# Kernel tuning notes

Hardware: AMD Instinct MI355X
Metric: run time of the kernel (lower is better)

Reference implementation:

```python
import jax, jax.numpy as jnp
import numpy as np

KS = 7          # kernel_size
DIL = 1         # dilation
NUM_ITER = 10   # num_iterations
K2 = KS * KS
CENTER = K2 // 2  # self position removed from window


def _sliding_window(x):
    # x: [B, C, H, W] -> [B, C, K2-1, H, W], replicate-padded local windows
    pad = (KS - 1) * DIL // 2
    B, C, H, W = x.shape
    xp = jnp.pad(x, ((0, 0), (0, 0), (pad, pad), (pad, pad)), mode='edge')
    wins = [xp[:, :, i * DIL:i * DIL + H, j * DIL:j * DIL + W]
            for i in range(KS) for j in range(KS)]
    wins = wins[:CENTER] + wins[CENTER + 1:]  # remove_self=True
    return jnp.stack(wins, axis=2)


def _local_affinity(x):
    # x: [B, C, H, W] -> softmax-normalized affinity [B, 1, K2-1, H, W]
    q = x[:, :, None]                 # [B, C, 1, H, W]
    k = _sliding_window(x)            # [B, C, K2-1, H, W]
    std = jnp.std(k, axis=2, keepdims=True, ddof=1)  # torch .std is unbiased
    aff = -jnp.abs(k - q) / (1e-8 + 0.1 * std)
    aff = jnp.mean(aff, axis=1, keepdims=True)       # [B, 1, K2-1, H, W]
    return jax.nn.softmax(aff, axis=2)


def setup_inputs() -> dict:
    key = jax.random.key(0)
    k1, k2 = jax.random.split(key)
    feats = jax.random.normal(k1, (4, 3, 128, 128), dtype=jnp.float32)
    mask = jax.random.uniform(k2, (4, 21, 128, 128), dtype=jnp.float32)
    return {"feats": feats, "mask": mask}


def reference(feats, mask):
    aff = _local_affinity(feats)  # [B, 1, K2-1, H, W]

    def body(m, _):
        v = _sliding_window(m)            # [B, Cm, K2-1, H, W]
        return (v * aff).sum(axis=2), None

    mask, _ = jax.lax.scan(body, mask, None, length=NUM_ITER)
    return mask
```

## Files before the change

### kernel.cpp

```cpp
#include <hip/hip_runtime.h>

constexpr int B   = 4;
constexpr int CF  = 3;
constexpr int CM  = 21;
constexpr int H   = 128;
constexpr int W   = 128;
constexpr int KS  = 7;
constexpr int PAD = 3;
constexpr int CENTER = (KS * KS) / 2;
constexpr int NNB = KS * KS - 1;
constexpr int NUM_ITER = 10;

constexpr int TILE = 16;
constexpr int TH   = TILE + 2 * PAD;
constexpr int TS   = 24;
constexpr int HW   = H * W;

constexpr int IN   = TILE + 4 * PAD;
constexpr int IND  = 15;
constexpr int MD   = 22;
constexpr int MDD  = 12;
constexpr int CPB  = 7;
constexpr int INP  = CPB * IN * IND;
constexpr int MDP  = CPB * MD * MDD;

__device__ __forceinline__ unsigned short f2b(float v) {
    unsigned int x = __float_as_uint(v);
    x += 0x7fffu + ((x >> 16) & 1u);
    return (unsigned short)(x >> 16);
}
__device__ __forceinline__ float blo(unsigned int d) { return __uint_as_float(d << 16); }
__device__ __forceinline__ float bhi(unsigned int d) { return __uint_as_float(d & 0xffff0000u); }

__global__ __launch_bounds__(256) void aff_kernel(const float* __restrict__ feats,
                                                  float* __restrict__ aff) {
    __shared__ float tile[CF][TH][TS];
    const int tx = threadIdx.x, ty = threadIdx.y;
    const int bx = blockIdx.x * TILE, by = blockIdx.y * TILE;
    const int b  = blockIdx.z;
    const int tid = ty * TILE + tx;

    for (int c = 0; c < CF; ++c) {
        const float* src = feats + (size_t)(b * CF + c) * HW;
        for (int idx = tid; idx < TH * TH; idx += 256) {
            const int r  = idx / TH, cc = idx - r * TH;
            const int gh = min(max(by + r  - PAD, 0), H - 1);
            const int gw = min(max(bx + cc - PAD, 0), W - 1);
            tile[c][r][cc] = src[gh * W + gw];
        }
    }
    __syncthreads();

    float q[CF], inv[CF];
    #pragma unroll
    for (int c = 0; c < CF; ++c) {
        const float* tp = &tile[c][ty][tx];
        q[c] = tp[PAD * TS + PAD];
        float s = 0.f, s2 = 0.f;
        #pragma unroll
        for (int i = 0; i < KS; ++i)
            #pragma unroll
            for (int j = 0; j < KS; ++j) {
                if (i == PAD && j == PAD) continue;
                const float v = tp[i * TS + j];
                s += v; s2 += v * v;
            }
        const float mean = s * (1.0f / NNB);
        const float var  = fmaxf(s2 - (float)NNB * mean * mean, 0.f) * (1.0f / (NNB - 1));
        inv[c] = 1.0f / (1e-8f + 0.1f * sqrtf(var));
    }

    float a[NNB];
    float mx = -1e30f;
    #pragma unroll
    for (int i = 0; i < KS; ++i)
        #pragma unroll
        for (int j = 0; j < KS; ++j) {
            const int nn = i * KS + j;
            if (nn == CENTER) continue;
            const int n = (nn < CENTER) ? nn : nn - 1;
            float t = 0.f;
            #pragma unroll
            for (int c = 0; c < CF; ++c)
                t += fabsf(tile[c][ty + i][tx + j] - q[c]) * inv[c];
            a[n] = -t * (1.0f / CF);
            mx = fmaxf(mx, a[n]);
        }
    float ssum = 0.f;
    #pragma unroll
    for (int n = 0; n < NNB; ++n) { a[n] = __expf(a[n] - mx); ssum += a[n]; }
    const float rs = 1.0f / ssum;

    const int h = by + ty, w = bx + tx;
    #pragma unroll
    for (int n = 0; n < NNB; ++n)
        aff[(((size_t)b * NNB + n) * H + h) * W + w] = a[n] * rs;
}

__global__ __launch_bounds__(256, 3) void fuse2_kernel(const float* __restrict__ mi,
                                                       const float* __restrict__ aff,
                                                       float* __restrict__ mo) {
    __shared__ unsigned int in_u[2 * INP];
    __shared__ unsigned int md_u[2 * MDP];

    const int tx = threadIdx.x, ty = threadIdx.y;
    const int tid = ty * TILE + tx;
    const int bx = blockIdx.x * TILE, by = blockIdx.y * TILE;
    const int zz = blockIdx.z;
    const int b  = zz / 3, g = zz % 3;
    const int c0 = g * CPB;

    const float* ab = aff + (size_t)b * NNB * HW;

    const int t2 = min(tid, 227);
    int rr_, qq_;
    if (t2 < 66)       { rr_ = t2 / MD;                    qq_ = t2 - rr_ * MD; }
    else if (t2 < 132) { const int s = t2 - 66;  rr_ = 19 + s / MD; qq_ = s % MD; }
    else               { const int s = t2 - 132; rr_ = 3 + s / 6;
                         const int u = s % 6;    qq_ = (u < 3) ? u : 16 + u; }
    const int gh_r = min(max(by - PAD + rr_, 0), H - 1);
    const int gw_r = min(max(bx - PAD + qq_, 0), W - 1);

    float a[NNB];
    {
        const float* ap = ab + (size_t)gh_r * W + gw_r;
        #pragma unroll
        for (int n = 0; n < NNB; ++n) a[n] = ap[(size_t)n * HW];
    }

    {
        const float* src = mi + (size_t)(b * CM + c0) * HW;
        for (int s = tid; s < IN * IN; s += 256) {
            const int rr = s / IN, qq = s - rr * IN;
            const int ih = min(max(by - 2 * PAD + rr, 0), H - 1);
            const int iw = min(max(bx - 2 * PAD + qq, 0), W - 1);
            const int go = ih * W + iw;
            #pragma unroll
            for (int c = 0; c < CPB; ++c) {
                const unsigned short v = f2b(src[c * HW + go]);
                unsigned short* rowA = (unsigned short*)&in_u[(c * IN + rr) * IND];
                unsigned short* rowB = (unsigned short*)&in_u[INP + (c * IN + rr) * IND];
                rowA[qq] = v;
                if (qq >= 1) rowB[qq - 1] = v;
            }
        }
    }
    __syncthreads();

    {
        const int ar = gh_r - by + PAD;
        const int ac = gw_r - bx + PAD;
        const int psel = (ac & 1) ? INP : 0;
        const int k0 = ac >> 1;
        const bool wr = (tid < 228);
        #pragma unroll
        for (int c = 0; c < CPB; ++c) {
            float s = 0.f;
            #pragma unroll
            for (int i = 0; i < KS; ++i) {
                const unsigned int* rp = &in_u[psel + (c * IN + ar + i) * IND + k0];
                const unsigned int d0 = rp[0], d1 = rp[1], d2 = rp[2], d3 = rp[3];
                const float wv[7] = { blo(d0), bhi(d0), blo(d1), bhi(d1),
                                      blo(d2), bhi(d2), blo(d3) };
                #pragma unroll
                for (int j = 0; j < KS; ++j) {
                    const int nn = i * KS + j;
                    if (nn == CENTER) continue;
                    const int n = (nn < CENTER) ? nn : nn - 1;
                    s += a[n] * wv[j];
                }
            }
            if (wr) {
                const unsigned short v = f2b(s);
                ((unsigned short*)&md_u[(c * MD + rr_) * MDD])[qq_] = v;
                if (qq_ >= 1)
                    ((unsigned short*)&md_u[MDP + (c * MD + rr_) * MDD])[qq_ - 1] = v;
            }
        }
    }

    {
        const float* ap = ab + (size_t)(by + ty) * W + (bx + tx);
        #pragma unroll
        for (int n = 0; n < NNB; ++n) a[n] = ap[(size_t)n * HW];
    }
    {
        const int ar = ty + PAD, ac = tx + PAD;
        const int psel = (ac & 1) ? INP : 0;
        const int k0 = ac >> 1;
        const int mq = tx + PAD;
        #pragma unroll
        for (int c = 0; c < CPB; ++c) {
            float s = 0.f;
            #pragma unroll
            for (int i = 0; i < KS; ++i) {
                const unsigned int* rp = &in_u[psel + (c * IN + ar + i) * IND + k0];
                const unsigned int d0 = rp[0], d1 = rp[1], d2 = rp[2], d3 = rp[3];
                const float wv[7] = { blo(d0), bhi(d0), blo(d1), bhi(d1),
                                      blo(d2), bhi(d2), blo(d3) };
                #pragma unroll
                for (int j = 0; j < KS; ++j) {
                    const int nn = i * KS + j;
                    if (nn == CENTER) continue;
                    const int n = (nn < CENTER) ? nn : nn - 1;
                    s += a[n] * wv[j];
                }
            }
            const unsigned short v = f2b(s);
            ((unsigned short*)&md_u[(c * MD + ty + PAD) * MDD])[mq] = v;
            ((unsigned short*)&md_u[MDP + (c * MD + ty + PAD) * MDD])[mq - 1] = v;
        }
    }
    __syncthreads();

    {
        const int psel = (tx & 1) ? MDP : 0;
        const int k0 = tx >> 1;
        float* dp = mo + (size_t)(b * CM + c0) * HW + (size_t)(by + ty) * W + (bx + tx);
        #pragma unroll
        for (int c = 0; c < CPB; ++c) {
            float s = 0.f;
            #pragma unroll
            for (int i = 0; i < KS; ++i) {
                const unsigned int* rp = &md_u[psel + (c * MD + ty + i) * MDD + k0];
                const unsigned int d0 = rp[0], d1 = rp[1], d2 = rp[2], d3 = rp[3];
                const float wv[7] = { blo(d0), bhi(d0), blo(d1), bhi(d1),
                                      blo(d2), bhi(d2), blo(d3) };
                #pragma unroll
                for (int j = 0; j < KS; ++j) {
                    const int nn = i * KS + j;
                    if (nn == CENTER) continue;
                    const int n = (nn < CENTER) ? nn : nn - 1;
                    s += a[n] * wv[j];
                }
            }
            dp[(size_t)c * HW] = s;
        }
    }
}

extern "C" void kernel_launch(void* const* d_in, const int* in_sizes, int n_in,
                              void* d_out, int out_size, void* d_ws, size_t ws_size,
                              hipStream_t stream) {
    const float* feats = (const float*)d_in[0];
    const float* mask  = (const float*)d_in[1];
    float* out = (float*)d_out;

    float* aff  = (float*)d_ws;
    float* buf0 = aff  + (size_t)B * NNB * HW;
    float* buf1 = buf0 + (size_t)B * CM  * HW;

    aff_kernel<<<dim3(W / TILE, H / TILE, B), dim3(TILE, TILE), 0, stream>>>(feats, aff);

    dim3 grid(W / TILE, H / TILE, B * 3);
    dim3 blk(TILE, TILE);
    fuse2_kernel<<<grid, blk, 0, stream>>>(mask, aff, buf0);
    fuse2_kernel<<<grid, blk, 0, stream>>>(buf0, aff, buf1);
    fuse2_kernel<<<grid, blk, 0, stream>>>(buf1, aff, buf0);
    fuse2_kernel<<<grid, blk, 0, stream>>>(buf0, aff, buf1);
    fuse2_kernel<<<grid, blk, 0, stream>>>(buf1, aff, out);
}
```

Measured before the change: 160.6 us.

## Use fp16 packed dot2 with parity-shifted weights instead of dual-copy bf16 tiles

Intermediate mask tiles in shared memory move from bf16 to fp16. The two parity-shifted copies of each tile are dropped. Each thread now builds per-row fp16 weight pairs, shifted by its column parity, so one unaligned-agnostic copy can be read and accumulated with v_dot2 (fdot2) instructions, about four per row instead of seven scalar FMAs. This halves shared-memory footprint and stores and cuts ALU work, at the cost of fp16 weights and activations (range and precision risk) and extra registers for the packed weights.

```diff
diff --git a/kernel.cpp b/kernel.cpp
--- a/kernel.cpp
+++ b/kernel.cpp
@@ -21,16 +21,22 @@
 constexpr int MD   = 22;
 constexpr int MDD  = 12;
 constexpr int CPB  = 7;
-constexpr int INP  = CPB * IN * IND;
-constexpr int MDP  = CPB * MD * MDD;
-
-__device__ __forceinline__ unsigned short f2b(float v) {
-    unsigned int x = __float_as_uint(v);
-    x += 0x7fffu + ((x >> 16) & 1u);
-    return (unsigned short)(x >> 16);
-}
-__device__ __forceinline__ float blo(unsigned int d) { return __uint_as_float(d << 16); }
-__device__ __forceinline__ float bhi(unsigned int d) { return __uint_as_float(d & 0xffff0000u); }
+
+typedef _Float16 h2 __attribute__((ext_vector_type(2)));
+
+__device__ __forceinline__ unsigned short f2h(float v) {
+    _Float16 h = (_Float16)v;
+    return __builtin_bit_cast(unsigned short, h);
+}
+__device__ __forceinline__ float hlo(unsigned int d) {
+    h2 p = __builtin_bit_cast(h2, d); return (float)p.x;
+}
+__device__ __forceinline__ float hhi(unsigned int d) {
+    h2 p = __builtin_bit_cast(h2, d); return (float)p.y;
+}
+
+#define WIJ(i, j) ((((i) * KS + (j)) == CENTER) ? 0.f : \
+    a[(((i) * KS + (j)) < CENTER) ? ((i) * KS + (j)) : ((i) * KS + (j) - 1)])
 
 __global__ __launch_bounds__(256) void aff_kernel(const float* __restrict__ feats,
                                                   float* __restrict__ aff) {
@@ -100,8 +106,8 @@
 __global__ __launch_bounds__(256, 3) void fuse2_kernel(const float* __restrict__ mi,
                                                        const float* __restrict__ aff,
                                                        float* __restrict__ mo) {
-    __shared__ unsigned int in_u[2 * INP];
-    __shared__ unsigned int md_u[2 * MDP];
+    __shared__ unsigned int in_u[CPB][IN][IND];
+    __shared__ unsigned int md_u[CPB][MD][MDD];
 
     const int tx = threadIdx.x, ty = threadIdx.y;
     const int tid = ty * TILE + tx;
@@ -111,6 +117,55 @@
     const int c0 = g * CPB;
 
     const float* ab = aff + (size_t)b * NNB * HW;
+
+#if __has_builtin(__builtin_amdgcn_fdot2)
+    h2 hw[KS][4];
+    #define BUILD_W(par)                                                     \
+        _Pragma("unroll")                                                    \
+        for (int i = 0; i < KS; ++i) {                                       \
+            float awk[8];                                                    \
+            _Pragma("unroll")                                                \
+            for (int k = 0; k < 8; ++k) {                                    \
+                const float w0 = (k < 7)  ? WIJ(i, k)     : 0.f;             \
+                const float w1 = (k >= 1) ? WIJ(i, k - 1) : 0.f;             \
+                awk[k] = (par) ? w1 : w0;                                    \
+            }                                                                \
+            _Pragma("unroll")                                                \
+            for (int m = 0; m < 4; ++m) {                                    \
+                h2 t; t.x = (_Float16)awk[2 * m]; t.y = (_Float16)awk[2 * m + 1]; \
+                hw[i][m] = t;                                                \
+            }                                                                \
+        }
+    #define ROW_DOT(s, rp, i)                                                \
+        do {                                                                 \
+            const unsigned int d0 = (rp)[0], d1 = (rp)[1],                   \
+                               d2 = (rp)[2], d3 = (rp)[3];                   \
+            s = __builtin_amdgcn_fdot2(hw[i][0], __builtin_bit_cast(h2, d0), s, false); \
+            s = __builtin_amdgcn_fdot2(hw[i][1], __builtin_bit_cast(h2, d1), s, false); \
+            s = __builtin_amdgcn_fdot2(hw[i][2], __builtin_bit_cast(h2, d2), s, false); \
+            s = __builtin_amdgcn_fdot2(hw[i][3], __builtin_bit_cast(h2, d3), s, false); \
+        } while (0)
+#else
+    float fw[KS][8];
+    #define BUILD_W(par)                                                     \
+        _Pragma("unroll")                                                    \
+        for (int i = 0; i < KS; ++i)                                         \
+            _Pragma("unroll")                                                \
+            for (int k = 0; k < 8; ++k) {                                    \
+                const float w0 = (k < 7)  ? WIJ(i, k)     : 0.f;             \
+                const float w1 = (k >= 1) ? WIJ(i, k - 1) : 0.f;             \
+                fw[i][k] = (par) ? w1 : w0;                                  \
+            }
+    #define ROW_DOT(s, rp, i)                                                \
+        do {                                                                 \
+            const unsigned int d0 = (rp)[0], d1 = (rp)[1],                   \
+                               d2 = (rp)[2], d3 = (rp)[3];                   \
+            s += fw[i][0] * hlo(d0) + fw[i][1] * hhi(d0)                     \
+               + fw[i][2] * hlo(d1) + fw[i][3] * hhi(d1)                     \
+               + fw[i][4] * hlo(d2) + fw[i][5] * hhi(d2)                     \
+               + fw[i][6] * hlo(d3) + fw[i][7] * hhi(d3);                    \
+        } while (0)
+#endif
 
     const int t2 = min(tid, 227);
     int rr_, qq_;
@@ -136,13 +191,8 @@
             const int iw = min(max(bx - 2 * PAD + qq, 0), W - 1);
             const int go = ih * W + iw;
             #pragma unroll
-            for (int c = 0; c < CPB; ++c) {
-                const unsigned short v = f2b(src[c * HW + go]);
-                unsigned short* rowA = (unsigned short*)&in_u[(c * IN + rr) * IND];
-                unsigned short* rowB = (unsigned short*)&in_u[INP + (c * IN + rr) * IND];
-                rowA[qq] = v;
-                if (qq >= 1) rowB[qq - 1] = v;
-            }
+            for (int c = 0; c < CPB; ++c)
+                ((unsigned short*)&in_u[c][rr][0])[qq] = f2h(src[c * HW + go]);
         }
     }
     __syncthreads();
@@ -150,32 +200,19 @@
     {
         const int ar = gh_r - by + PAD;
         const int ac = gw_r - bx + PAD;
-        const int psel = (ac & 1) ? INP : 0;
         const int k0 = ac >> 1;
+        const int par = ac & 1;
+        BUILD_W(par);
         const bool wr = (tid < 228);
         #pragma unroll
         for (int c = 0; c < CPB; ++c) {
             float s = 0.f;
             #pragma unroll
             for (int i = 0; i < KS; ++i) {
-                const unsigned int* rp = &in_u[psel + (c * IN + ar + i) * IND + k0];
-                const unsigned int d0 = rp[0], d1 = rp[1], d2 = rp[2], d3 = rp[3];
-                const float wv[7] = { blo(d0), bhi(d0), blo(d1), bhi(d1),
-                                      blo(d2), bhi(d2), blo(d3) };
-                #pragma unroll
-                for (int j = 0; j < KS; ++j) {
-                    const int nn = i * KS + j;
-                    if (nn == CENTER) continue;
-                    const int n = (nn < CENTER) ? nn : nn - 1;
-                    s += a[n] * wv[j];
-                }
-            }
-            if (wr) {
-                const unsigned short v = f2b(s);
-                ((unsigned short*)&md_u[(c * MD + rr_) * MDD])[qq_] = v;
-                if (qq_ >= 1)
-                    ((unsigned short*)&md_u[MDP + (c * MD + rr_) * MDD])[qq_ - 1] = v;
-            }
+                const unsigned int* rp = &in_u[c][ar + i][k0];
+                ROW_DOT(s, rp, i);
+            }
+            if (wr) ((unsigned short*)&md_u[c][rr_][0])[qq_] = f2h(s);
         }
     }
 
@@ -186,53 +223,34 @@
     }
     {
         const int ar = ty + PAD, ac = tx + PAD;
-        const int psel = (ac & 1) ? INP : 0;
         const int k0 = ac >> 1;
-        const int mq = tx + PAD;
+        const int par = ac & 1;
+        BUILD_W(par);
         #pragma unroll
         for (int c = 0; c < CPB; ++c) {
             float s = 0.f;
             #pragma unroll
             for (int i = 0; i < KS; ++i) {
-                const unsigned int* rp = &in_u[psel + (c * IN + ar + i) * IND + k0];
-                const unsigned int d0 = rp[0], d1 = rp[1], d2 = rp[2], d3 = rp[3];
-                const float wv[7] = { blo(d0), bhi(d0), blo(d1), bhi(d1),
-                                      blo(d2), bhi(d2), blo(d3) };
-                #pragma unroll
-                for (int j = 0; j < KS; ++j) {
-                    const int nn = i * KS + j;
-                    if (nn == CENTER) continue;
-                    const int n = (nn < CENTER) ? nn : nn - 1;
-                    s += a[n] * wv[j];
-                }
-            }
-            const unsigned short v = f2b(s);
-            ((unsigned short*)&md_u[(c * MD + ty + PAD) * MDD])[mq] = v;
-            ((unsigned short*)&md_u[MDP + (c * MD + ty + PAD) * MDD])[mq - 1] = v;
+                const unsigned int* rp = &in_u[c][ar + i][k0];
+                ROW_DOT(s, rp, i);
+            }
+            ((unsigned short*)&md_u[c][ty + PAD][0])[tx + PAD] = f2h(s);
         }
     }
     __syncthreads();
 
     {
-        const int psel = (tx & 1) ? MDP : 0;
         const int k0 = tx >> 1;
+        const int par = tx & 1;
+        BUILD_W(par);
         float* dp = mo + (size_t)(b * CM + c0) * HW + (size_t)(by + ty) * W + (bx + tx);
         #pragma unroll
         for (int c = 0; c < CPB; ++c) {
             float s = 0.f;
             #pragma unroll
             for (int i = 0; i < KS; ++i) {
-                const unsigned int* rp = &md_u[psel + (c * MD + ty + i) * MDD + k0];
-                const unsigned int d0 = rp[0], d1 = rp[1], d2 = rp[2], d3 = rp[3];
-                const float wv[7] = { blo(d0), bhi(d0), blo(d1), bhi(d1),
-                                      blo(d2), bhi(d2), blo(d3) };
-                #pragma unroll
-                for (int j = 0; j < KS; ++j) {
-                    const int nn = i * KS + j;
-                    if (nn == CENTER) continue;
-                    const int n = (nn < CENTER) ? nn : nn - 1;
-                    s += a[n] * wv[j];
-                }
+                const unsigned int* rp = &md_u[c][ty + i][k0];
+                ROW_DOT(s, rp, i);
             }
             dp[(size_t)c * HW] = s;
         }
```

New measurement: 132.7 us. 17.4% less time.
